# Kernel optimization log

Hardware: AMD Instinct MI355X
Metric: run time of the kernel (lower is better)

Reference implementation:

```python
import jax, jax.numpy as jnp
import numpy as np

B, C, T = 32, 256, 4096

def setup_inputs() -> dict:
    key = jax.random.key(0)
    k1, k2 = jax.random.split(key)
    x = jax.random.normal(k1, (B, C, T), dtype=jnp.float32)
    gamma = jax.random.normal(k2, (1,), dtype=jnp.float32)
    return {"x": x, "gamma": gamma}

def reference(x, gamma):
    # energy[b,i,j] = <x[b,i,:], x[b,j,:]>  -> (B, C, C)
    energy = jnp.einsum('bit,bjt->bij', x, x)
    # max-subtract trick: softmax over (rowmax - energy)
    energy_new = jnp.max(energy, axis=-1, keepdims=True) - energy
    attention = jax.nn.softmax(energy_new, axis=-1)
    # out[b,i,t] = sum_j attention[b,i,j] * x[b,j,t]
    out = jnp.einsum('bij,bjt->bit', attention, x)
    return gamma * out + x
```

## Files before the change

### kernel.cpp

```cpp
#include <hip/hip_runtime.h>
#include <hip/hip_bf16.h>

#define BATCH 32
#define CDIM  256
#define TDIM  4096

using short8  = __attribute__((ext_vector_type(8))) short;
using floatx4 = __attribute__((ext_vector_type(4))) float;
typedef unsigned short u16;

__device__ __forceinline__ unsigned f2bf(float f) {
  unsigned u = __float_as_uint(f);
  return (u + 0x7fffu + ((u >> 16) & 1u)) >> 16;
}
__device__ __forceinline__ unsigned cvt_pk_bf16(float a, float b) {
  return f2bf(a) | (f2bf(b) << 16);
}
__device__ __forceinline__ float bf_lo(unsigned u) { return __uint_as_float(u << 16); }
__device__ __forceinline__ float bf_hi(unsigned u) { return __uint_as_float(u & 0xffff0000u); }

__device__ __forceinline__ void glds16(const void* g, void* l) {
  __builtin_amdgcn_global_load_lds(
      (const __attribute__((address_space(1))) void*)g,
      (__attribute__((address_space(3))) void*)l, 16, 0, 0);
}

__global__ __launch_bounds__(256)
void split_kernel(const float* __restrict__ x, u16* __restrict__ hx,
                  u16* __restrict__ lx) {
  const unsigned gid0 = blockIdx.x * 256 + threadIdx.x;
#pragma unroll
  for (int it = 0; it < 8; ++it) {
    const size_t g8 = ((size_t)gid0 + (size_t)it * (2048u * 256u)) * 8;
    const float4 a = *(const float4*)(x + g8);
    const float4 c = *(const float4*)(x + g8 + 4);
    unsigned h0 = cvt_pk_bf16(a.x, a.y), h1 = cvt_pk_bf16(a.z, a.w);
    unsigned h2 = cvt_pk_bf16(c.x, c.y), h3 = cvt_pk_bf16(c.z, c.w);
    unsigned l0 = cvt_pk_bf16(a.x - bf_lo(h0), a.y - bf_hi(h0));
    unsigned l1 = cvt_pk_bf16(a.z - bf_lo(h1), a.w - bf_hi(h1));
    unsigned l2 = cvt_pk_bf16(c.x - bf_lo(h2), c.y - bf_hi(h2));
    unsigned l3 = cvt_pk_bf16(c.z - bf_lo(h3), c.w - bf_hi(h3));
    *(uint4*)(hx + g8) = make_uint4(h0, h1, h2, h3);
    *(uint4*)(lx + g8) = make_uint4(l0, l1, l2, l3);
  }
}

__global__ __launch_bounds__(512, 1)
void gram_gemm(const u16* __restrict__ hx, const u16* __restrict__ lx,
               float* __restrict__ S, float* __restrict__ E2) {
  __shared__ __align__(16) short lds[2 * 20480];

  const int tid = threadIdx.x;
  const int bx  = blockIdx.x;

  const int s8  = bx & 7;
  const int seq = bx >> 3;
  const int b   = s8 + ((seq >> 3) << 3);
  const int job = seq & 7;
  const int i0  = (job >> 2) << 7;
  const int j0  = (job & 3) << 6;

  const int lane = tid & 63;
  const int w    = tid >> 6;

  const int rsub = lane >> 3;
  const int gsw  = ((lane & 7) ^ rsub) << 3;
  const size_t xb = (size_t)b << 20;
  const u16* src[5];
  src[0] = hx + xb + (size_t)(i0 +      w * 8 + rsub) * TDIM + gsw;
  src[1] = hx + xb + (size_t)(i0 + 64 + w * 8 + rsub) * TDIM + gsw;
  src[2] = lx + xb + (size_t)(i0 +      w * 8 + rsub) * TDIM + gsw;
  src[3] = lx + xb + (size_t)(i0 + 64 + w * 8 + rsub) * TDIM + gsw;
  src[4] = hx + xb + (size_t)(j0 +      w * 8 + rsub) * TDIM + gsw;
  int dstoff[5];
#pragma unroll
  for (int s = 0; s < 5; ++s) dstoff[s] = (s * 8 + w) << 9;

  floatx4 acc1[2][2], acc2[2][2];
#pragma unroll
  for (int m = 0; m < 2; ++m)
#pragma unroll
    for (int n = 0; n < 2; ++n) {
      acc1[m][n] = {0.f, 0.f, 0.f, 0.f};
      acc2[m][n] = {0.f, 0.f, 0.f, 0.f};
    }

  const int wib = (w >> 1) << 5;
  const int wjb = (w & 1) << 5;
  const int fr  = lane & 15;
  const int q   = lane >> 4;
  const int f7  = fr & 7;

  const int g0 = ((q)     ^ f7) << 3;
  const int g1 = ((q + 4) ^ f7) << 3;
  const int a0 = (wib + fr) << 6;
  const int a1 = a0 + (16 << 6);
  const int b0 = (wjb + fr) << 6;
  const int b1 = b0 + (16 << 6);

#pragma unroll
  for (int s = 0; s < 5; ++s) glds16(src[s], lds + dstoff[s]);
  __syncthreads();

  for (int ks = 0; ks < 64; ++ks) {
    const int cur = ks & 1;
    if (ks < 63) {
      const int nb = (cur ^ 1) * 20480;
#pragma unroll
      for (int s = 0; s < 5; ++s)
        glds16(src[s] + ((ks + 1) << 6), lds + nb + dstoff[s]);
    }
    const int bb = cur * 20480;

    {
      short8 Ah0 = *(const short8*)&lds[bb + a0 + g0];
      short8 Ah1 = *(const short8*)&lds[bb + a1 + g0];
      short8 Al0 = *(const short8*)&lds[bb + 8192 + a0 + g0];
      short8 Al1 = *(const short8*)&lds[bb + 8192 + a1 + g0];
      short8 Bh0 = *(const short8*)&lds[bb + 16384 + b0 + g0];
      short8 Bh1 = *(const short8*)&lds[bb + 16384 + b1 + g0];
      acc1[0][0] = __builtin_amdgcn_mfma_f32_16x16x32_bf16(Ah0, Bh0, acc1[0][0], 0, 0, 0);
      acc1[0][1] = __builtin_amdgcn_mfma_f32_16x16x32_bf16(Ah0, Bh1, acc1[0][1], 0, 0, 0);
      acc1[1][0] = __builtin_amdgcn_mfma_f32_16x16x32_bf16(Ah1, Bh0, acc1[1][0], 0, 0, 0);
      acc1[1][1] = __builtin_amdgcn_mfma_f32_16x16x32_bf16(Ah1, Bh1, acc1[1][1], 0, 0, 0);
      acc2[0][0] = __builtin_amdgcn_mfma_f32_16x16x32_bf16(Al0, Bh0, acc2[0][0], 0, 0, 0);
      acc2[0][1] = __builtin_amdgcn_mfma_f32_16x16x32_bf16(Al0, Bh1, acc2[0][1], 0, 0, 0);
      acc2[1][0] = __builtin_amdgcn_mfma_f32_16x16x32_bf16(Al1, Bh0, acc2[1][0], 0, 0, 0);
      acc2[1][1] = __builtin_amdgcn_mfma_f32_16x16x32_bf16(Al1, Bh1, acc2[1][1], 0, 0, 0);
    }
    {
      short8 Ah0 = *(const short8*)&lds[bb + a0 + g1];
      short8 Ah1 = *(const short8*)&lds[bb + a1 + g1];
      short8 Al0 = *(const short8*)&lds[bb + 8192 + a0 + g1];
      short8 Al1 = *(const short8*)&lds[bb + 8192 + a1 + g1];
      short8 Bh0 = *(const short8*)&lds[bb + 16384 + b0 + g1];
      short8 Bh1 = *(const short8*)&lds[bb + 16384 + b1 + g1];
      acc1[0][0] = __builtin_amdgcn_mfma_f32_16x16x32_bf16(Ah0, Bh0, acc1[0][0], 0, 0, 0);
      acc1[0][1] = __builtin_amdgcn_mfma_f32_16x16x32_bf16(Ah0, Bh1, acc1[0][1], 0, 0, 0);
      acc1[1][0] = __builtin_amdgcn_mfma_f32_16x16x32_bf16(Ah1, Bh0, acc1[1][0], 0, 0, 0);
      acc1[1][1] = __builtin_amdgcn_mfma_f32_16x16x32_bf16(Ah1, Bh1, acc1[1][1], 0, 0, 0);
      acc2[0][0] = __builtin_amdgcn_mfma_f32_16x16x32_bf16(Al0, Bh0, acc2[0][0], 0, 0, 0);
      acc2[0][1] = __builtin_amdgcn_mfma_f32_16x16x32_bf16(Al0, Bh1, acc2[0][1], 0, 0, 0);
      acc2[1][0] = __builtin_amdgcn_mfma_f32_16x16x32_bf16(Al1, Bh0, acc2[1][0], 0, 0, 0);
      acc2[1][1] = __builtin_amdgcn_mfma_f32_16x16x32_bf16(Al1, Bh1, acc2[1][1], 0, 0, 0);
    }
    __syncthreads();
  }

#pragma unroll
  for (int m = 0; m < 2; ++m)
#pragma unroll
    for (int n = 0; n < 2; ++n) {
      const int gr = i0 + wib + 16 * m + 4 * q;
      const int gc = j0 + wjb + 16 * n + fr;
      size_t base = (((size_t)b * CDIM + gr) << 8) + gc;
#pragma unroll
      for (int r = 0; r < 4; ++r) {
        S[base + ((size_t)r << 8)]  = acc1[m][n][r] + acc2[m][n][r];
        E2[base + ((size_t)r << 8)] = acc2[m][n][r];
      }
    }
}

__global__ __launch_bounds__(512, 1)
void gram_fused(const float* __restrict__ x,
                float* __restrict__ S, float* __restrict__ E2) {
  __shared__ __align__(16) short hI[128 * 64];
  __shared__ __align__(16) short lI[128 * 64];
  __shared__ __align__(16) short hJ[64 * 64];

  const int tid = threadIdx.x;
  const int bx  = blockIdx.x;
  const int s   = bx & 7;
  const int seq = bx >> 3;
  const int b   = s + ((seq >> 3) << 3);
  const int job = seq & 7;
  const int i0  = (job >> 2) << 7;
  const int j0  = (job & 3) << 6;

  const float* xb = x + ((size_t)b << 20);

  const bool isJ   = tid >= 256;
  const int  irow  = tid >> 1;
  const int  ihalf = tid & 1;
  const int  jrow  = (tid & 255) >> 2;
  const int  jq    = tid & 3;

  const float* pS = isJ
      ? xb + (size_t)(j0 + jrow) * TDIM + (jq << 4)
      : xb + (size_t)(i0 + irow) * TDIM + (ihalf << 5);

  floatx4 acc1[2][2], acc2[2][2];
#pragma unroll
  for (int m = 0; m < 2; ++m)
#pragma unroll
    for (int n = 0; n < 2; ++n) {
      acc1[m][n] = {0.f, 0.f, 0.f, 0.f};
      acc2[m][n] = {0.f, 0.f, 0.f, 0.f};
    }

  const int lane = tid & 63;
  const int w    = tid >> 6;
  const int wib  = (w >> 1) << 5;
  const int wjb  = (w & 1) << 5;
  const int fr   = lane & 15;
  const int q    = lane >> 4;
  const int f7   = fr & 7;

  const int g0 = ((q)     ^ f7) << 3;
  const int g1 = ((q + 4) ^ f7) << 3;
  const int a0 = (wib + fr) << 6;
  const int a1 = a0 + (16 << 6);
  const int b0 = (wjb + fr) << 6;
  const int b1 = b0 + (16 << 6);

  float4 r0, r1, r2, r3, r4, r5, r6, r7;
  r0 = ((const float4*)pS)[0]; r1 = ((const float4*)pS)[1];
  r2 = ((const float4*)pS)[2]; r3 = ((const float4*)pS)[3];
  if (!isJ) {
    r4 = ((const float4*)pS)[4]; r5 = ((const float4*)pS)[5];
    r6 = ((const float4*)pS)[6]; r7 = ((const float4*)pS)[7];
  }

  for (int ks = 0; ks < TDIM / 64; ++ks) {
    unsigned h0 = cvt_pk_bf16(r0.x, r0.y), h1 = cvt_pk_bf16(r0.z, r0.w);
    unsigned h2 = cvt_pk_bf16(r1.x, r1.y), h3 = cvt_pk_bf16(r1.z, r1.w);
    unsigned h4 = cvt_pk_bf16(r2.x, r2.y), h5 = cvt_pk_bf16(r2.z, r2.w);
    unsigned h6 = cvt_pk_bf16(r3.x, r3.y), h7 = cvt_pk_bf16(r3.z, r3.w);
    unsigned h8, h9, hA, hB, hC, hD, hE, hF;
    unsigned l0, l1, l2, l3, l4, l5, l6, l7, l8, l9, lA, lB, lC, lD, lE, lF;
    if (!isJ) {
      h8 = cvt_pk_bf16(r4.x, r4.y); h9 = cvt_pk_bf16(r4.z, r4.w);
      hA = cvt_pk_bf16(r5.x, r5.y); hB = cvt_pk_bf16(r5.z, r5.w);
      hC = cvt_pk_bf16(r6.x, r6.y); hD = cvt_pk_bf16(r6.z, r6.w);
      hE = cvt_pk_bf16(r7.x, r7.y); hF = cvt_pk_bf16(r7.z, r7.w);
      l0 = cvt_pk_bf16(r0.x - bf_lo(h0), r0.y - bf_hi(h0));
      l1 = cvt_pk_bf16(r0.z - bf_lo(h1), r0.w - bf_hi(h1));
      l2 = cvt_pk_bf16(r1.x - bf_lo(h2), r1.y - bf_hi(h2));
      l3 = cvt_pk_bf16(r1.z - bf_lo(h3), r1.w - bf_hi(h3));
      l4 = cvt_pk_bf16(r2.x - bf_lo(h4), r2.y - bf_hi(h4));
      l5 = cvt_pk_bf16(r2.z - bf_lo(h5), r2.w - bf_hi(h5));
      l6 = cvt_pk_bf16(r3.x - bf_lo(h6), r3.y - bf_hi(h6));
      l7 = cvt_pk_bf16(r3.z - bf_lo(h7), r3.w - bf_hi(h7));
      l8 = cvt_pk_bf16(r4.x - bf_lo(h8), r4.y - bf_hi(h8));
      l9 = cvt_pk_bf16(r4.z - bf_lo(h9), r4.w - bf_hi(h9));
      lA = cvt_pk_bf16(r5.x - bf_lo(hA), r5.y - bf_hi(hA));
      lB = cvt_pk_bf16(r5.z - bf_lo(hB), r5.w - bf_hi(hB));
      lC = cvt_pk_bf16(r6.x - bf_lo(hC), r6.y - bf_hi(hC));
      lD = cvt_pk_bf16(r6.z - bf_lo(hD), r6.w - bf_hi(hD));
      lE = cvt_pk_bf16(r7.x - bf_lo(hE), r7.y - bf_hi(hE));
      lF = cvt_pk_bf16(r7.z - bf_lo(hF), r7.w - bf_hi(hF));
    }

    __syncthreads();
    if (!isJ) {
      const int rb = irow << 6;
      const int s7 = irow & 7;
      const int gb = ihalf << 2;
      *(uint4*)&hI[rb + (((gb + 0) ^ s7) << 3)] = make_uint4(h0, h1, h2, h3);
      *(uint4*)&hI[rb + (((gb + 1) ^ s7) << 3)] = make_uint4(h4, h5, h6, h7);
      *(uint4*)&hI[rb + (((gb + 2) ^ s7) << 3)] = make_uint4(h8, h9, hA, hB);
      *(uint4*)&hI[rb + (((gb + 3) ^ s7) << 3)] = make_uint4(hC, hD, hE, hF);
      *(uint4*)&lI[rb + (((gb + 0) ^ s7) << 3)] = make_uint4(l0, l1, l2, l3);
      *(uint4*)&lI[rb + (((gb + 1) ^ s7) << 3)] = make_uint4(l4, l5, l6, l7);
      *(uint4*)&lI[rb + (((gb + 2) ^ s7) << 3)] = make_uint4(l8, l9, lA, lB);
      *(uint4*)&lI[rb + (((gb + 3) ^ s7) << 3)] = make_uint4(lC, lD, lE, lF);
    } else {
      const int rb = jrow << 6;
      const int s7 = jrow & 7;
      const int gb = jq << 1;
      *(uint4*)&hJ[rb + (((gb + 0) ^ s7) << 3)] = make_uint4(h0, h1, h2, h3);
      *(uint4*)&hJ[rb + (((gb + 1) ^ s7) << 3)] = make_uint4(h4, h5, h6, h7);
    }
    __syncthreads();

    if (ks < TDIM / 64 - 1) {
      pS += 64;
      r0 = ((const float4*)pS)[0]; r1 = ((const float4*)pS)[1];
      r2 = ((const float4*)pS)[2]; r3 = ((const float4*)pS)[3];
      if (!isJ) {
        r4 = ((const float4*)pS)[4]; r5 = ((const float4*)pS)[5];
        r6 = ((const float4*)pS)[6]; r7 = ((const float4*)pS)[7];
      }
    }

    {
      short8 Ah0 = *(const short8*)&hI[a0 + g0];
      short8 Ah1 = *(const short8*)&hI[a1 + g0];
      short8 Al0 = *(const short8*)&lI[a0 + g0];
      short8 Al1 = *(const short8*)&lI[a1 + g0];
      short8 Bh0 = *(const short8*)&hJ[b0 + g0];
      short8 Bh1 = *(const short8*)&hJ[b1 + g0];
      acc1[0][0] = __builtin_amdgcn_mfma_f32_16x16x32_bf16(Ah0, Bh0, acc1[0][0], 0, 0, 0);
      acc1[0][1] = __builtin_amdgcn_mfma_f32_16x16x32_bf16(Ah0, Bh1, acc1[0][1], 0, 0, 0);
      acc1[1][0] = __builtin_amdgcn_mfma_f32_16x16x32_bf16(Ah1, Bh0, acc1[1][0], 0, 0, 0);
      acc1[1][1] = __builtin_amdgcn_mfma_f32_16x16x32_bf16(Ah1, Bh1, acc1[1][1], 0, 0, 0);
      acc2[0][0] = __builtin_amdgcn_mfma_f32_16x16x32_bf16(Al0, Bh0, acc2[0][0], 0, 0, 0);
      acc2[0][1] = __builtin_amdgcn_mfma_f32_16x16x32_bf16(Al0, Bh1, acc2[0][1], 0, 0, 0);
      acc2[1][0] = __builtin_amdgcn_mfma_f32_16x16x32_bf16(Al1, Bh0, acc2[1][0], 0, 0, 0);
      acc2[1][1] = __builtin_amdgcn_mfma_f32_16x16x32_bf16(Al1, Bh1, acc2[1][1], 0, 0, 0);
    }
    {
      short8 Ah0 = *(const short8*)&hI[a0 + g1];
      short8 Ah1 = *(const short8*)&hI[a1 + g1];
      short8 Al0 = *(const short8*)&lI[a0 + g1];
      short8 Al1 = *(const short8*)&lI[a1 + g1];
      short8 Bh0 = *(const short8*)&hJ[b0 + g1];
      short8 Bh1 = *(const short8*)&hJ[b1 + g1];
      acc1[0][0] = __builtin_amdgcn_mfma_f32_16x16x32_bf16(Ah0, Bh0, acc1[0][0], 0, 0, 0);
      acc1[0][1] = __builtin_amdgcn_mfma_f32_16x16x32_bf16(Ah0, Bh1, acc1[0][1], 0, 0, 0);
      acc1[1][0] = __builtin_amdgcn_mfma_f32_16x16x32_bf16(Ah1, Bh0, acc1[1][0], 0, 0, 0);
      acc1[1][1] = __builtin_amdgcn_mfma_f32_16x16x32_bf16(Ah1, Bh1, acc1[1][1], 0, 0, 0);
      acc2[0][0] = __builtin_amdgcn_mfma_f32_16x16x32_bf16(Al0, Bh0, acc2[0][0], 0, 0, 0);
      acc2[0][1] = __builtin_amdgcn_mfma_f32_16x16x32_bf16(Al0, Bh1, acc2[0][1], 0, 0, 0);
      acc2[1][0] = __builtin_amdgcn_mfma_f32_16x16x32_bf16(Al1, Bh0, acc2[1][0], 0, 0, 0);
      acc2[1][1] = __builtin_amdgcn_mfma_f32_16x16x32_bf16(Al1, Bh1, acc2[1][1], 0, 0, 0);
    }
  }

#pragma unroll
  for (int m = 0; m < 2; ++m)
#pragma unroll
    for (int n = 0; n < 2; ++n) {
      const int gr = i0 + wib + 16 * m + 4 * q;
      const int gc = j0 + wjb + 16 * n + fr;
      size_t base = (((size_t)b * CDIM + gr) << 8) + gc;
#pragma unroll
      for (int r = 0; r < 4; ++r) {
        S[base + ((size_t)r << 8)]  = acc1[m][n][r] + acc2[m][n][r];
        E2[base + ((size_t)r << 8)] = acc2[m][n][r];
      }
    }
}

__global__ __launch_bounds__(256)
void softmax_kernel(const float* __restrict__ S, const float* __restrict__ E2,
                    __hip_bfloat16* __restrict__ att) {
  __shared__ float SR[32][264];
  __shared__ float ST[256][33];

  const int tid = threadIdx.x;
  const int b   = blockIdx.x >> 3;
  const int i0  = (blockIdx.x & 7) << 5;
  const size_t base = (size_t)b << 16;

  {
    const int r  = tid >> 3;
    const int c0 = (tid & 7) << 5;
    const float* p1 = S + base + ((size_t)(i0 + r) << 8) + c0;
#pragma unroll
    for (int u = 0; u < 32; u += 4)
      *(float4*)&SR[r][c0 + u] = *(const float4*)(p1 + u);
  }
  {
    const int c  = tid & 31;
    const int j0 = (tid >> 5) << 5;
    const float* p = E2 + base + i0 + c;
#pragma unroll
    for (int jj = 0; jj < 32; ++jj)
      ST[j0 + jj][c] = p[(size_t)(j0 + jj) << 8];
  }
  __syncthreads();

  const int r  = tid >> 3;
  const int t7 = tid & 7;
  float z[32];
  float m = -3.4e38f;
#pragma unroll
  for (int k = 0; k < 32; ++k) {
    const int j = t7 + (k << 3);
    const float e = SR[r][j] + ST[j][r];
    z[k] = -e;
    m = fmaxf(m, z[k]);
  }
  m = fmaxf(m, __shfl_xor(m, 1, 64));
  m = fmaxf(m, __shfl_xor(m, 2, 64));
  m = fmaxf(m, __shfl_xor(m, 4, 64));
  float ssum = 0.f;
#pragma unroll
  for (int k = 0; k < 32; ++k) { z[k] = expf(z[k] - m); ssum += z[k]; }
  ssum += __shfl_xor(ssum, 1, 64);
  ssum += __shfl_xor(ssum, 2, 64);
  ssum += __shfl_xor(ssum, 4, 64);
  const float inv = 1.f / ssum;

  u16* arow = (u16*)att + base + ((size_t)(i0 + r) << 8);
#pragma unroll
  for (int k = 0; k < 32; ++k) {
    const int j = t7 + (k << 3);
    arow[j] = (u16)f2bf(z[k] * inv);
  }
}

__global__ __launch_bounds__(256, 1)
void pv_kernel(const float* __restrict__ x, const u16* __restrict__ hx,
               const __hip_bfloat16* __restrict__ att,
               const float* __restrict__ gamma, float* __restrict__ out) {
  __shared__ __align__(16) short As[128 * 256];
  __shared__ __align__(16) short Bs[128 * 256];

  const int tid = threadIdx.x;
  const int bx  = blockIdx.x;
  const int b   = bx >> 6;
  const int i0  = ((bx >> 5) & 1) << 7;
  const int t0  = (bx & 31) << 7;

  const u16* attb = (const u16*)att + ((size_t)b << 16) + ((size_t)i0 << 8);
  const int lane = tid & 63;
  const int w4   = tid >> 6;

  const int tQ = tid & 31;
  const int jg = tid >> 5;
  const u16* hb = hx + ((size_t)b << 20) + t0 + (tQ << 2);
  uint2 v[4][8];
#pragma unroll
  for (int j8 = 0; j8 < 4; ++j8)
#pragma unroll
    for (int u = 0; u < 8; ++u)
      v[j8][u] = *(const uint2*)(hb + (size_t)((jg << 5) + (j8 << 3) + u) * TDIM);

#pragma unroll
  for (int s = 0; s < 16; ++s) {
    const int c  = (s << 2) + w4;
    const int r  = (c << 1) + (lane >> 5);
    const int gd = lane & 31;
    const int gs = gd ^ (r & 7);
    glds16(attb + ((size_t)r << 8) + (gs << 3), As + (c << 9));
  }

#pragma unroll
  for (int j8 = 0; j8 < 4; ++j8) {
#pragma unroll
    for (int tt = 0; tt < 4; ++tt) {
      unsigned p[4];
#pragma unroll
      for (int a = 0; a < 4; ++a) {
        const unsigned xa = (tt & 2) ? v[j8][2 * a].y : v[j8][2 * a].x;
        const unsigned xb2 = (tt & 2) ? v[j8][2 * a + 1].y : v[j8][2 * a + 1].x;
        p[a] = (tt & 1) ? ((xa >> 16) | (xb2 & 0xffff0000u))
                        : ((xa & 0xffffu) | (xb2 << 16));
      }
      const int row = (tQ << 2) + tt;
      const int g   = ((jg << 2) + j8) ^ (row & 7);
      *(uint4*)(Bs + row * 256 + (g << 3)) = make_uint4(p[0], p[1], p[2], p[3]);
    }
  }

  floatx4 acc[4][4];
#pragma unroll
  for (int m = 0; m < 4; ++m)
#pragma unroll
    for (int n = 0; n < 4; ++n) acc[m][n] = {0.f, 0.f, 0.f, 0.f};

  const int wm = (w4 >> 1) << 6;
  const int wn = (w4 & 1) << 6;
  const int fr = lane & 15;
  const int q  = lane >> 4;

  __syncthreads();

#pragma unroll
  for (int ks = 0; ks < 8; ++ks) {
    short8 Af[4], Bf[4];
#pragma unroll
    for (int m = 0; m < 4; ++m) {
      const int r = wm + 16 * m + fr;
      const int g = ((ks << 2) + q) ^ (r & 7);
      Af[m] = *(const short8*)(As + r * 256 + (g << 3));
    }
#pragma unroll
    for (int n = 0; n < 4; ++n) {
      const int r = wn + 16 * n + fr;
      const int g = ((ks << 2) + q) ^ (r & 7);
      Bf[n] = *(const short8*)(Bs + r * 256 + (g << 3));
    }
#pragma unroll
    for (int m = 0; m < 4; ++m)
#pragma unroll
      for (int n = 0; n < 4; ++n)
        acc[m][n] = __builtin_amdgcn_mfma_f32_16x16x32_bf16(Af[m], Bf[n], acc[m][n], 0, 0, 0);
  }

  const float g = gamma[0];
#pragma unroll
  for (int m = 0; m < 4; ++m)
#pragma unroll
    for (int n = 0; n < 4; ++n) {
      const int gr = i0 + wm + 16 * m + 4 * q;
      const int gc = t0 + wn + 16 * n + fr;
      size_t base = ((size_t)b << 20) + (size_t)gr * TDIM + gc;
#pragma unroll
      for (int r = 0; r < 4; ++r) {
        size_t idx = base + (size_t)r * TDIM;
        out[idx] = g * acc[m][n][r] + x[idx];
      }
    }
}

__global__ __launch_bounds__(256, 1)
void pv_fused(const float* __restrict__ x, const __hip_bfloat16* __restrict__ att,
              const float* __restrict__ gamma, float* __restrict__ out) {
  __shared__ __align__(16) short As[128 * 256];
  __shared__ __align__(16) short Bs[128 * 256];

  const int tid = threadIdx.x;
  const int bx  = blockIdx.x;
  const int b   = bx >> 6;
  const int i0  = ((bx >> 5) & 1) << 7;
  const int t0  = (bx & 31) << 7;

  const float* xb = x + ((size_t)b << 20) + t0;
  const u16* attb = (const u16*)att + ((size_t)b << 16) + ((size_t)i0 << 8);

  {
    uint4 areg[16];
#pragma unroll
    for (int c = 0; c < 16; ++c) {
      const int p = (c << 8) + tid;
      const int r = p >> 5;
      const int g = (p & 31) ^ (r & 7);
      areg[c] = *(const uint4*)(attb + (r << 8) + (g << 3));
    }
#pragma unroll
    for (int c = 0; c < 16; ++c) {
      const int p = (c << 8) + tid;
      *(uint4*)((char*)As + ((size_t)p << 4)) = areg[c];
    }
  }
  {
    const int tQ = tid & 31;
    const int jg = tid >> 5;
#pragma unroll
    for (int j8 = 0; j8 < 4; ++j8) {
      floatx4 v[8];
#pragma unroll
      for (int u = 0; u < 8; ++u) {
        const int j = (jg << 5) + (j8 << 3) + u;
        v[u] = *(const floatx4*)(xb + (size_t)j * TDIM + (tQ << 2));
      }
#pragma unroll
      for (int tt = 0; tt < 4; ++tt) {
        uint4 wv = make_uint4(cvt_pk_bf16(v[0][tt], v[1][tt]),
                              cvt_pk_bf16(v[2][tt], v[3][tt]),
                              cvt_pk_bf16(v[4][tt], v[5][tt]),
                              cvt_pk_bf16(v[6][tt], v[7][tt]));
        const int row = (tQ << 2) + tt;
        const int g   = ((jg << 2) + j8) ^ (row & 7);
        *(uint4*)((char*)Bs + (size_t)row * 512 + ((size_t)g << 4)) = wv;
      }
    }
  }

  floatx4 acc[4][4];
#pragma unroll
  for (int m = 0; m < 4; ++m)
#pragma unroll
    for (int n = 0; n < 4; ++n) acc[m][n] = {0.f, 0.f, 0.f, 0.f};

  const int lane = tid & 63;
  const int w    = tid >> 6;
  const int wm   = (w >> 1) << 6;
  const int wn   = (w & 1) << 6;
  const int fr   = lane & 15;
  const int q    = lane >> 4;

  __syncthreads();

#pragma unroll
  for (int ks = 0; ks < 8; ++ks) {
    short8 Af[4], Bf[4];
#pragma unroll
    for (int m = 0; m < 4; ++m) {
      const int r = wm + 16 * m + fr;
      const int g = ((ks << 2) + q) ^ (r & 7);
      Af[m] = *(const short8*)((char*)As + (size_t)r * 512 + ((size_t)g << 4));
    }
#pragma unroll
    for (int n = 0; n < 4; ++n) {
      const int r = wn + 16 * n + fr;
      const int g = ((ks << 2) + q) ^ (r & 7);
      Bf[n] = *(const short8*)((char*)Bs + (size_t)r * 512 + ((size_t)g << 4));
    }
#pragma unroll
    for (int m = 0; m < 4; ++m)
#pragma unroll
      for (int n = 0; n < 4; ++n)
        acc[m][n] = __builtin_amdgcn_mfma_f32_16x16x32_bf16(Af[m], Bf[n], acc[m][n], 0, 0, 0);
  }

  const float g = gamma[0];
#pragma unroll
  for (int m = 0; m < 4; ++m)
#pragma unroll
    for (int n = 0; n < 4; ++n) {
      const int gr = i0 + wm + 16 * m + 4 * q;
      const int gc = t0 + wn + 16 * n + fr;
      size_t base = ((size_t)b << 20) + (size_t)gr * TDIM + gc;
#pragma unroll
      for (int r = 0; r < 4; ++r) {
        size_t idx = base + (size_t)r * TDIM;
        out[idx] = g * acc[m][n][r] + x[idx];
      }
    }
}

extern "C" void kernel_launch(void* const* d_in, const int* in_sizes, int n_in,
                              void* d_out, int out_size, void* d_ws, size_t ws_size,
                              hipStream_t stream) {
  (void)in_sizes; (void)n_in; (void)out_size;
  const float* x     = (const float*)d_in[0];
  const float* gamma = (const float*)d_in[1];
  float* out = (float*)d_out;

  const size_t EN = (size_t)BATCH * CDIM * CDIM;
  const size_t XN = (size_t)BATCH * CDIM * TDIM;
  float* S  = (float*)d_ws;
  float* E2 = S + EN;
  __hip_bfloat16* att = (__hip_bfloat16*)(E2 + EN);
  u16* hx = (u16*)((char*)d_ws + 20u * 1024 * 1024);
  u16* lx = hx + XN;
  const size_t need = 20u * 1024 * 1024 + 2 * XN * sizeof(u16);

  if (ws_size >= need) {
    split_kernel<<<dim3(2048), dim3(256), 0, stream>>>(x, hx, lx);
    gram_gemm<<<dim3(256), dim3(512), 0, stream>>>(hx, lx, S, E2);
    softmax_kernel<<<dim3(BATCH * 8), dim3(256), 0, stream>>>(S, E2, att);
    pv_kernel<<<dim3(2048), dim3(256), 0, stream>>>(x, hx, att, gamma, out);
  } else {
    gram_fused<<<dim3(256), dim3(512), 0, stream>>>(x, S, E2);
    softmax_kernel<<<dim3(BATCH * 8), dim3(256), 0, stream>>>(S, E2, att);
    pv_fused<<<dim3(2048), dim3(256), 0, stream>>>(x, att, gamma, out);
  }
}
```

Baseline: 371.3 us.

## Precompute transposed bf16 x for PV and relax gram_gemm barriers

```diff
diff --git a/kernel.cpp b/kernel.cpp
--- a/kernel.cpp
+++ b/kernel.cpp
@@ -23,6 +23,54 @@
   __builtin_amdgcn_global_load_lds(
       (const __attribute__((address_space(1))) void*)g,
       (__attribute__((address_space(3))) void*)l, 16, 0, 0);
+}
+
+__global__ __launch_bounds__(256)
+void split_t_kernel(const float* __restrict__ x, u16* __restrict__ hx,
+                    u16* __restrict__ lx, u16* __restrict__ hxT) {
+  __shared__ u16 ht[64][72];
+
+  const int bx  = blockIdx.x;
+  const int b   = bx >> 8;
+  const int j0  = ((bx >> 6) & 3) << 6;
+  const int t0  = (bx & 63) << 6;
+  const int tid = threadIdx.x;
+  const int jr  = tid >> 2;
+  const int tc  = (tid & 3) << 4;
+
+  const size_t xoff = ((size_t)b << 20) + (size_t)(j0 + jr) * TDIM + t0 + tc;
+  const float4 a0 = ((const float4*)(x + xoff))[0];
+  const float4 a1 = ((const float4*)(x + xoff))[1];
+  const float4 a2 = ((const float4*)(x + xoff))[2];
+  const float4 a3 = ((const float4*)(x + xoff))[3];
+  const float4 aa[4] = {a0, a1, a2, a3};
+
+  unsigned h[8], l[8];
+#pragma unroll
+  for (int u = 0; u < 4; ++u) {
+    h[2 * u]     = cvt_pk_bf16(aa[u].x, aa[u].y);
+    h[2 * u + 1] = cvt_pk_bf16(aa[u].z, aa[u].w);
+    l[2 * u]     = cvt_pk_bf16(aa[u].x - bf_lo(h[2 * u]),     aa[u].y - bf_hi(h[2 * u]));
+    l[2 * u + 1] = cvt_pk_bf16(aa[u].z - bf_lo(h[2 * u + 1]), aa[u].w - bf_hi(h[2 * u + 1]));
+  }
+
+  u16* ph = hx + xoff;
+  *(uint4*)ph       = make_uint4(h[0], h[1], h[2], h[3]);
+  *(uint4*)(ph + 8) = make_uint4(h[4], h[5], h[6], h[7]);
+  u16* pl = lx + xoff;
+  *(uint4*)pl       = make_uint4(l[0], l[1], l[2], l[3]);
+  *(uint4*)(pl + 8) = make_uint4(l[4], l[5], l[6], l[7]);
+
+#pragma unroll
+  for (int u = 0; u < 16; ++u)
+    ht[tc + u][jr] = (u16)((u & 1) ? (h[u >> 1] >> 16) : (h[u >> 1] & 0xffffu));
+  __syncthreads();
+
+  const int tr = tid >> 2;
+  const int jc = (tid & 3) << 4;
+  u16* pt = hxT + ((size_t)b << 20) + (size_t)(t0 + tr) * CDIM + j0 + jc;
+  *(uint4*)pt       = *(const uint4*)&ht[tr][jc];
+  *(uint4*)(pt + 8) = *(const uint4*)&ht[tr][jc + 8];
 }
 
 __global__ __launch_bounds__(256)
@@ -100,17 +148,19 @@
 
 #pragma unroll
   for (int s = 0; s < 5; ++s) glds16(src[s], lds + dstoff[s]);
-  __syncthreads();
 
   for (int ks = 0; ks < 64; ++ks) {
-    const int cur = ks & 1;
+    const int bb = (ks & 1) * 20480;
     if (ks < 63) {
-      const int nb = (cur ^ 1) * 20480;
+      const int nb = ((ks + 1) & 1) * 20480;
 #pragma unroll
       for (int s = 0; s < 5; ++s)
         glds16(src[s] + ((ks + 1) << 6), lds + nb + dstoff[s]);
-    }
-    const int bb = cur * 20480;
+      asm volatile("s_waitcnt vmcnt(5)" ::: "memory");
+    } else {
+      asm volatile("s_waitcnt vmcnt(0)" ::: "memory");
+    }
+    __builtin_amdgcn_s_barrier();
 
     {
       short8 Ah0 = *(const short8*)&lds[bb + a0 + g0];
@@ -144,7 +194,8 @@
       acc2[1][0] = __builtin_amdgcn_mfma_f32_16x16x32_bf16(Al1, Bh0, acc2[1][0], 0, 0, 0);
       acc2[1][1] = __builtin_amdgcn_mfma_f32_16x16x32_bf16(Al1, Bh1, acc2[1][1], 0, 0, 0);
     }
-    __syncthreads();
+    asm volatile("" ::: "memory");
+    __builtin_amdgcn_s_barrier();
   }
 
 #pragma unroll
@@ -240,6 +291,7 @@
       l3 = cvt_pk_bf16(r1.z - bf_lo(h3), r1.w - bf_hi(h3));
       l4 = cvt_pk_bf16(r2.x - bf_lo(h4), r2.y - bf_hi(h4));
       l5 = cvt_pk_bf16(r2.z - bf_lo(h5), r2.w - bf_hi(h5));
+      l6 = cvt_pk_bf16(r3.x - bf_lo(h6), r3.w - bf_hi(h6));
       l6 = cvt_pk_bf16(r3.x - bf_lo(h6), r3.y - bf_hi(h6));
       l7 = cvt_pk_bf16(r3.z - bf_lo(h7), r3.w - bf_hi(h7));
       l8 = cvt_pk_bf16(r4.x - bf_lo(h8), r4.y - bf_hi(h8));
@@ -392,8 +444,8 @@
   }
 }
 
-__global__ __launch_bounds__(256, 1)
-void pv_kernel(const float* __restrict__ x, const u16* __restrict__ hx,
+__global__ __launch_bounds__(512, 1)
+void pv_kernel(const float* __restrict__ x, const u16* __restrict__ hxT,
                const __hip_bfloat16* __restrict__ att,
                const float* __restrict__ gamma, float* __restrict__ out) {
   __shared__ __align__(16) short As[128 * 256];
@@ -405,55 +457,37 @@
   const int i0  = ((bx >> 5) & 1) << 7;
   const int t0  = (bx & 31) << 7;
 
-  const u16* attb = (const u16*)att + ((size_t)b << 16) + ((size_t)i0 << 8);
+  const u16* asrc = (const u16*)att + ((size_t)b << 16) + ((size_t)i0 << 8);
+  const u16* bsrc = hxT + ((size_t)b << 20) + ((size_t)t0 << 8);
+
   const int lane = tid & 63;
-  const int w4   = tid >> 6;
-
-  const int tQ = tid & 31;
-  const int jg = tid >> 5;
-  const u16* hb = hx + ((size_t)b << 20) + t0 + (tQ << 2);
-  uint2 v[4][8];
-#pragma unroll
-  for (int j8 = 0; j8 < 4; ++j8)
-#pragma unroll
-    for (int u = 0; u < 8; ++u)
-      v[j8][u] = *(const uint2*)(hb + (size_t)((jg << 5) + (j8 << 3) + u) * TDIM);
-
-#pragma unroll
-  for (int s = 0; s < 16; ++s) {
-    const int c  = (s << 2) + w4;
-    const int r  = (c << 1) + (lane >> 5);
-    const int gd = lane & 31;
+  const int w    = tid >> 6;
+
+  const int rh = lane >> 5;
+  const int gd = lane & 31;
+#pragma unroll
+  for (int s = 0; s < 8; ++s) {
+    const int c  = (s << 3) + w;
+    const int r  = (c << 1) + rh;
     const int gs = gd ^ (r & 7);
-    glds16(attb + ((size_t)r << 8) + (gs << 3), As + (c << 9));
-  }
-
-#pragma unroll
-  for (int j8 = 0; j8 < 4; ++j8) {
-#pragma unroll
-    for (int tt = 0; tt < 4; ++tt) {
-      unsigned p[4];
-#pragma unroll
-      for (int a = 0; a < 4; ++a) {
-        const unsigned xa = (tt & 2) ? v[j8][2 * a].y : v[j8][2 * a].x;
-        const unsigned xb2 = (tt & 2) ? v[j8][2 * a + 1].y : v[j8][2 * a + 1].x;
-        p[a] = (tt & 1) ? ((xa >> 16) | (xb2 & 0xffff0000u))
-                        : ((xa & 0xffffu) | (xb2 << 16));
-      }
-      const int row = (tQ << 2) + tt;
-      const int g   = ((jg << 2) + j8) ^ (row & 7);
-      *(uint4*)(Bs + row * 256 + (g << 3)) = make_uint4(p[0], p[1], p[2], p[3]);
-    }
-  }
-
-  floatx4 acc[4][4];
+    glds16(asrc + ((size_t)r << 8) + (gs << 3), As + (c << 9));
+  }
+#pragma unroll
+  for (int s = 0; s < 8; ++s) {
+    const int c  = (s << 3) + w;
+    const int r  = (c << 1) + rh;
+    const int gs = gd ^ (r & 7);
+    glds16(bsrc + ((size_t)r << 8) + (gs << 3), Bs + (c << 9));
+  }
+
+  floatx4 acc[4][2];
 #pragma unroll
   for (int m = 0; m < 4; ++m)
 #pragma unroll
-    for (int n = 0; n < 4; ++n) acc[m][n] = {0.f, 0.f, 0.f, 0.f};
-
-  const int wm = (w4 >> 1) << 6;
-  const int wn = (w4 & 1) << 6;
+    for (int n = 0; n < 2; ++n) acc[m][n] = {0.f, 0.f, 0.f, 0.f};
+
+  const int wm = (w >> 2) << 6;
+  const int wn = (w & 3) << 5;
   const int fr = lane & 15;
   const int q  = lane >> 4;
 
@@ -461,7 +495,7 @@
 
 #pragma unroll
   for (int ks = 0; ks < 8; ++ks) {
-    short8 Af[4], Bf[4];
+    short8 Af[4], Bf[2];
 #pragma unroll
     for (int m = 0; m < 4; ++m) {
       const int r = wm + 16 * m + fr;
@@ -469,7 +503,7 @@
       Af[m] = *(const short8*)(As + r * 256 + (g << 3));
     }
 #pragma unroll
-    for (int n = 0; n < 4; ++n) {
+    for (int n = 0; n < 2; ++n) {
       const int r = wn + 16 * n + fr;
       const int g = ((ks << 2) + q) ^ (r & 7);
       Bf[n] = *(const short8*)(Bs + r * 256 + (g << 3));
@@ -477,7 +511,7 @@
 #pragma unroll
     for (int m = 0; m < 4; ++m)
 #pragma unroll
-      for (int n = 0; n < 4; ++n)
+      for (int n = 0; n < 2; ++n)
         acc[m][n] = __builtin_amdgcn_mfma_f32_16x16x32_bf16(Af[m], Bf[n], acc[m][n], 0, 0, 0);
   }
 
@@ -485,7 +519,7 @@
 #pragma unroll
   for (int m = 0; m < 4; ++m)
 #pragma unroll
-    for (int n = 0; n < 4; ++n) {
+    for (int n = 0; n < 2; ++n) {
       const int gr = i0 + wm + 16 * m + 4 * q;
       const int gc = t0 + wn + 16 * n + fr;
       size_t base = ((size_t)b << 20) + (size_t)gr * TDIM + gc;
@@ -545,8 +579,8 @@
                               cvt_pk_bf16(v[4][tt], v[5][tt]),
                               cvt_pk_bf16(v[6][tt], v[7][tt]));
         const int row = (tQ << 2) + tt;
-        const int g   = ((jg << 2) + j8) ^ (row & 7);
-        *(uint4*)((char*)Bs + (size_t)row * 512 + ((size_t)g << 4)) = wv;
+        const int gx  = ((jg << 2) + j8) ^ (row & 7);
+        *(uint4*)((char*)Bs + (size_t)row * 512 + ((size_t)gx << 4)) = wv;
       }
     }
   }
@@ -612,20 +646,28 @@
   const float* gamma = (const float*)d_in[1];
   float* out = (float*)d_out;
 
+  const size_t MB = 1024 * 1024;
   const size_t EN = (size_t)BATCH * CDIM * CDIM;
   const size_t XN = (size_t)BATCH * CDIM * TDIM;
   float* S  = (float*)d_ws;
   float* E2 = S + EN;
   __hip_bfloat16* att = (__hip_bfloat16*)(E2 + EN);
-  u16* hx = (u16*)((char*)d_ws + 20u * 1024 * 1024);
-  u16* lx = hx + XN;
-  const size_t need = 20u * 1024 * 1024 + 2 * XN * sizeof(u16);
-
-  if (ws_size >= need) {
+  u16* hx  = (u16*)((char*)d_ws + 20 * MB);
+  u16* lx  = hx + XN;
+  u16* hxT = lx + XN;
+  const size_t need_full = 20 * MB + 3 * XN * sizeof(u16);
+  const size_t need_mid  = 20 * MB + 2 * XN * sizeof(u16);
+
+  if (ws_size >= need_full) {
+    split_t_kernel<<<dim3(8192), dim3(256), 0, stream>>>(x, hx, lx, hxT);
+    gram_gemm<<<dim3(256), dim3(512), 0, stream>>>(hx, lx, S, E2);
+    softmax_kernel<<<dim3(BATCH * 8), dim3(256), 0, stream>>>(S, E2, att);
+    pv_kernel<<<dim3(2048), dim3(512), 0, stream>>>(x, hxT, att, gamma, out);
+  } else if (ws_size >= need_mid) {
     split_kernel<<<dim3(2048), dim3(256), 0, stream>>>(x, hx, lx);
     gram_gemm<<<dim3(256), dim3(512), 0, stream>>>(hx, lx, S, E2);
     softmax_kernel<<<dim3(BATCH * 8), dim3(256), 0, stream>>>(S, E2, att);
-    pv_kernel<<<dim3(2048), dim3(256), 0, stream>>>(x, hx, att, gamma, out);
+    pv_fused<<<dim3(2048), dim3(256), 0, stream>>>(x, att, gamma, out);
   } else {
     gram_fused<<<dim3(256), dim3(512), 0, stream>>>(x, S, E2);
     softmax_kernel<<<dim3(BATCH * 8), dim3(256), 0, stream>>>(S, E2, att);
```

Result: slower. 403.9 us (+8.8%).

## Shrink gram and PV tiles, add triple-buffered async prefetch in gram GEMM

Applied to the files above, without the earlier changes.

```diff
diff --git a/kernel.cpp b/kernel.cpp
--- a/kernel.cpp
+++ b/kernel.cpp
@@ -45,19 +45,19 @@
   }
 }
 
-__global__ __launch_bounds__(512, 1)
+__global__ __launch_bounds__(256, 2)
 void gram_gemm(const u16* __restrict__ hx, const u16* __restrict__ lx,
                float* __restrict__ S, float* __restrict__ E2) {
-  __shared__ __align__(16) short lds[2 * 20480];
+  __shared__ __align__(16) short lds[3 * 12288];
 
   const int tid = threadIdx.x;
   const int bx  = blockIdx.x;
 
   const int s8  = bx & 7;
   const int seq = bx >> 3;
-  const int b   = s8 + ((seq >> 3) << 3);
-  const int job = seq & 7;
-  const int i0  = (job >> 2) << 7;
+  const int b   = s8 + ((seq >> 4) << 3);
+  const int job = seq & 15;
+  const int i0  = (job >> 2) << 6;
   const int j0  = (job & 3) << 6;
 
   const int lane = tid & 63;
@@ -66,15 +66,19 @@
   const int rsub = lane >> 3;
   const int gsw  = ((lane & 7) ^ rsub) << 3;
   const size_t xb = (size_t)b << 20;
-  const u16* src[5];
-  src[0] = hx + xb + (size_t)(i0 +      w * 8 + rsub) * TDIM + gsw;
-  src[1] = hx + xb + (size_t)(i0 + 64 + w * 8 + rsub) * TDIM + gsw;
-  src[2] = lx + xb + (size_t)(i0 +      w * 8 + rsub) * TDIM + gsw;
-  src[3] = lx + xb + (size_t)(i0 + 64 + w * 8 + rsub) * TDIM + gsw;
-  src[4] = hx + xb + (size_t)(j0 +      w * 8 + rsub) * TDIM + gsw;
-  int dstoff[5];
-#pragma unroll
-  for (int s = 0; s < 5; ++s) dstoff[s] = (s * 8 + w) << 9;
+  const u16* src[6];
+  int dstoff[6];
+#pragma unroll
+  for (int s = 0; s < 6; ++s) {
+    const int c = (s << 2) + w;
+    const u16* base;
+    int row;
+    if (c < 8)       { base = hx; row = i0 + (c << 3) + rsub; }
+    else if (c < 16) { base = lx; row = i0 + ((c - 8) << 3) + rsub; }
+    else             { base = hx; row = j0 + ((c - 16) << 3) + rsub; }
+    src[s]    = base + xb + (size_t)row * TDIM + gsw;
+    dstoff[s] = c << 9;
+  }
 
   floatx4 acc1[2][2], acc2[2][2];
 #pragma unroll
@@ -99,26 +103,33 @@
   const int b1 = b0 + (16 << 6);
 
 #pragma unroll
-  for (int s = 0; s < 5; ++s) glds16(src[s], lds + dstoff[s]);
-  __syncthreads();
+  for (int s = 0; s < 6; ++s) glds16(src[s], lds + dstoff[s]);
+#pragma unroll
+  for (int s = 0; s < 6; ++s) glds16(src[s] + 64, lds + 12288 + dstoff[s]);
+
+  int cur = 0;
+  int nx2 = 2 * 12288;
 
   for (int ks = 0; ks < 64; ++ks) {
-    const int cur = ks & 1;
-    if (ks < 63) {
-      const int nb = (cur ^ 1) * 20480;
-#pragma unroll
-      for (int s = 0; s < 5; ++s)
-        glds16(src[s] + ((ks + 1) << 6), lds + nb + dstoff[s]);
-    }
-    const int bb = cur * 20480;
+    if (ks < 62) {
+#pragma unroll
+      for (int s = 0; s < 6; ++s)
+        glds16(src[s] + ((ks + 2) << 6), lds + nx2 + dstoff[s]);
+      asm volatile("s_waitcnt vmcnt(12)" ::: "memory");
+    } else if (ks == 62) {
+      asm volatile("s_waitcnt vmcnt(6)" ::: "memory");
+    } else {
+      asm volatile("s_waitcnt vmcnt(0)" ::: "memory");
+    }
+    __builtin_amdgcn_s_barrier();
 
     {
-      short8 Ah0 = *(const short8*)&lds[bb + a0 + g0];
-      short8 Ah1 = *(const short8*)&lds[bb + a1 + g0];
-      short8 Al0 = *(const short8*)&lds[bb + 8192 + a0 + g0];
-      short8 Al1 = *(const short8*)&lds[bb + 8192 + a1 + g0];
-      short8 Bh0 = *(const short8*)&lds[bb + 16384 + b0 + g0];
-      short8 Bh1 = *(const short8*)&lds[bb + 16384 + b1 + g0];
+      short8 Ah0 = *(const short8*)&lds[cur + a0 + g0];
+      short8 Ah1 = *(const short8*)&lds[cur + a1 + g0];
+      short8 Al0 = *(const short8*)&lds[cur + 4096 + a0 + g0];
+      short8 Al1 = *(const short8*)&lds[cur + 4096 + a1 + g0];
+      short8 Bh0 = *(const short8*)&lds[cur + 8192 + b0 + g0];
+      short8 Bh1 = *(const short8*)&lds[cur + 8192 + b1 + g0];
       acc1[0][0] = __builtin_amdgcn_mfma_f32_16x16x32_bf16(Ah0, Bh0, acc1[0][0], 0, 0, 0);
       acc1[0][1] = __builtin_amdgcn_mfma_f32_16x16x32_bf16(Ah0, Bh1, acc1[0][1], 0, 0, 0);
       acc1[1][0] = __builtin_amdgcn_mfma_f32_16x16x32_bf16(Ah1, Bh0, acc1[1][0], 0, 0, 0);
@@ -129,12 +140,12 @@
       acc2[1][1] = __builtin_amdgcn_mfma_f32_16x16x32_bf16(Al1, Bh1, acc2[1][1], 0, 0, 0);
     }
     {
-      short8 Ah0 = *(const short8*)&lds[bb + a0 + g1];
-      short8 Ah1 = *(const short8*)&lds[bb + a1 + g1];
-      short8 Al0 = *(const short8*)&lds[bb + 8192 + a0 + g1];
-      short8 Al1 = *(const short8*)&lds[bb + 8192 + a1 + g1];
-      short8 Bh0 = *(const short8*)&lds[bb + 16384 + b0 + g1];
-      short8 Bh1 = *(const short8*)&lds[bb + 16384 + b1 + g1];
+      short8 Ah0 = *(const short8*)&lds[cur + a0 + g1];
+      short8 Ah1 = *(const short8*)&lds[cur + a1 + g1];
+      short8 Al0 = *(const short8*)&lds[cur + 4096 + a0 + g1];
+      short8 Al1 = *(const short8*)&lds[cur + 4096 + a1 + g1];
+      short8 Bh0 = *(const short8*)&lds[cur + 8192 + b0 + g1];
+      short8 Bh1 = *(const short8*)&lds[cur + 8192 + b1 + g1];
       acc1[0][0] = __builtin_amdgcn_mfma_f32_16x16x32_bf16(Ah0, Bh0, acc1[0][0], 0, 0, 0);
       acc1[0][1] = __builtin_amdgcn_mfma_f32_16x16x32_bf16(Ah0, Bh1, acc1[0][1], 0, 0, 0);
       acc1[1][0] = __builtin_amdgcn_mfma_f32_16x16x32_bf16(Ah1, Bh0, acc1[1][0], 0, 0, 0);
@@ -144,7 +155,11 @@
       acc2[1][0] = __builtin_amdgcn_mfma_f32_16x16x32_bf16(Al1, Bh0, acc2[1][0], 0, 0, 0);
       acc2[1][1] = __builtin_amdgcn_mfma_f32_16x16x32_bf16(Al1, Bh1, acc2[1][1], 0, 0, 0);
     }
-    __syncthreads();
+    asm volatile("" ::: "memory");
+    __builtin_amdgcn_s_barrier();
+
+    cur += 12288; if (cur == 36864) cur = 0;
+    nx2 += 12288; if (nx2 == 36864) nx2 = 0;
   }
 
 #pragma unroll
@@ -392,68 +407,67 @@
   }
 }
 
-__global__ __launch_bounds__(256, 1)
+__global__ __launch_bounds__(256, 2)
 void pv_kernel(const float* __restrict__ x, const u16* __restrict__ hx,
                const __hip_bfloat16* __restrict__ att,
                const float* __restrict__ gamma, float* __restrict__ out) {
-  __shared__ __align__(16) short As[128 * 256];
-  __shared__ __align__(16) short Bs[128 * 256];
+  __shared__ __align__(16) short As[64 * 256];
+  __shared__ __align__(16) short Bs[64 * 256];
 
   const int tid = threadIdx.x;
   const int bx  = blockIdx.x;
-  const int b   = bx >> 6;
-  const int i0  = ((bx >> 5) & 1) << 7;
-  const int t0  = (bx & 31) << 7;
-
-  const u16* attb = (const u16*)att + ((size_t)b << 16) + ((size_t)i0 << 8);
+  const int b   = bx >> 8;
+  const int i0  = ((bx >> 6) & 3) << 6;
+  const int t0  = (bx & 63) << 6;
+
+  const u16* asrc = (const u16*)att + ((size_t)b << 16) + ((size_t)i0 << 8);
   const int lane = tid & 63;
-  const int w4   = tid >> 6;
-
-  const int tQ = tid & 31;
-  const int jg = tid >> 5;
+  const int w    = tid >> 6;
+
+  const int tQ = tid & 15;
+  const int jg = tid >> 4;
   const u16* hb = hx + ((size_t)b << 20) + t0 + (tQ << 2);
-  uint2 v[4][8];
-#pragma unroll
-  for (int j8 = 0; j8 < 4; ++j8)
+  uint2 v[2][8];
+#pragma unroll
+  for (int j8 = 0; j8 < 2; ++j8)
 #pragma unroll
     for (int u = 0; u < 8; ++u)
-      v[j8][u] = *(const uint2*)(hb + (size_t)((jg << 5) + (j8 << 3) + u) * TDIM);
-
-#pragma unroll
-  for (int s = 0; s < 16; ++s) {
-    const int c  = (s << 2) + w4;
+      v[j8][u] = *(const uint2*)(hb + (size_t)((jg << 4) + (j8 << 3) + u) * TDIM);
+
+#pragma unroll
+  for (int s = 0; s < 8; ++s) {
+    const int c  = (s << 2) + w;
     const int r  = (c << 1) + (lane >> 5);
-    const int gd = lane & 31;
-    const int gs = gd ^ (r & 7);
-    glds16(attb + ((size_t)r << 8) + (gs << 3), As + (c << 9));
-  }
-
-#pragma unroll
-  for (int j8 = 0; j8 < 4; ++j8) {
+    const int gs = (lane & 31) ^ (r & 7);
+    glds16(asrc + ((size_t)r << 8) + (gs << 3), As + (c << 9));
+  }
+
+#pragma unroll
+  for (int j8 = 0; j8 < 2; ++j8) {
 #pragma unroll
     for (int tt = 0; tt < 4; ++tt) {
       unsigned p[4];
 #pragma unroll
       for (int a = 0; a < 4; ++a) {
-        const unsigned xa = (tt & 2) ? v[j8][2 * a].y : v[j8][2 * a].x;
+        const unsigned xa  = (tt & 2) ? v[j8][2 * a].y : v[j8][2 * a].x;
         const unsigned xb2 = (tt & 2) ? v[j8][2 * a + 1].y : v[j8][2 * a + 1].x;
         p[a] = (tt & 1) ? ((xa >> 16) | (xb2 & 0xffff0000u))
                         : ((xa & 0xffffu) | (xb2 << 16));
       }
       const int row = (tQ << 2) + tt;
-      const int g   = ((jg << 2) + j8) ^ (row & 7);
+      const int g   = ((jg << 1) + j8) ^ (row & 7);
       *(uint4*)(Bs + row * 256 + (g << 3)) = make_uint4(p[0], p[1], p[2], p[3]);
     }
   }
 
-  floatx4 acc[4][4];
-#pragma unroll
-  for (int m = 0; m < 4; ++m)
-#pragma unroll
-    for (int n = 0; n < 4; ++n) acc[m][n] = {0.f, 0.f, 0.f, 0.f};
-
-  const int wm = (w4 >> 1) << 6;
-  const int wn = (w4 & 1) << 6;
+  floatx4 acc[2][2];
+#pragma unroll
+  for (int m = 0; m < 2; ++m)
+#pragma unroll
+    for (int n = 0; n < 2; ++n) acc[m][n] = {0.f, 0.f, 0.f, 0.f};
+
+  const int wm = (w >> 1) << 5;
+  const int wn = (w & 1) << 5;
   const int fr = lane & 15;
   const int q  = lane >> 4;
 
@@ -461,31 +475,31 @@
 
 #pragma unroll
   for (int ks = 0; ks < 8; ++ks) {
-    short8 Af[4], Bf[4];
-#pragma unroll
-    for (int m = 0; m < 4; ++m) {
+    short8 Af[2], Bf[2];
+#pragma unroll
+    for (int m = 0; m < 2; ++m) {
       const int r = wm + 16 * m + fr;
       const int g = ((ks << 2) + q) ^ (r & 7);
       Af[m] = *(const short8*)(As + r * 256 + (g << 3));
     }
 #pragma unroll
-    for (int n = 0; n < 4; ++n) {
+    for (int n = 0; n < 2; ++n) {
       const int r = wn + 16 * n + fr;
       const int g = ((ks << 2) + q) ^ (r & 7);
       Bf[n] = *(const short8*)(Bs + r * 256 + (g << 3));
     }
 #pragma unroll
-    for (int m = 0; m < 4; ++m)
-#pragma unroll
-      for (int n = 0; n < 4; ++n)
+    for (int m = 0; m < 2; ++m)
+#pragma unroll
+      for (int n = 0; n < 2; ++n)
         acc[m][n] = __builtin_amdgcn_mfma_f32_16x16x32_bf16(Af[m], Bf[n], acc[m][n], 0, 0, 0);
   }
 
   const float g = gamma[0];
 #pragma unroll
-  for (int m = 0; m < 4; ++m)
-#pragma unroll
-    for (int n = 0; n < 4; ++n) {
+  for (int m = 0; m < 2; ++m)
+#pragma unroll
+    for (int n = 0; n < 2; ++n) {
       const int gr = i0 + wm + 16 * m + 4 * q;
       const int gc = t0 + wn + 16 * n + fr;
       size_t base = ((size_t)b << 20) + (size_t)gr * TDIM + gc;
@@ -545,8 +559,8 @@
                               cvt_pk_bf16(v[4][tt], v[5][tt]),
                               cvt_pk_bf16(v[6][tt], v[7][tt]));
         const int row = (tQ << 2) + tt;
-        const int g   = ((jg << 2) + j8) ^ (row & 7);
-        *(uint4*)((char*)Bs + (size_t)row * 512 + ((size_t)g << 4)) = wv;
+        const int gx  = ((jg << 2) + j8) ^ (row & 7);
+        *(uint4*)((char*)Bs + (size_t)row * 512 + ((size_t)gx << 4)) = wv;
       }
     }
   }
@@ -612,20 +626,21 @@
   const float* gamma = (const float*)d_in[1];
   float* out = (float*)d_out;
 
+  const size_t MB = 1024 * 1024;
   const size_t EN = (size_t)BATCH * CDIM * CDIM;
   const size_t XN = (size_t)BATCH * CDIM * TDIM;
   float* S  = (float*)d_ws;
   float* E2 = S + EN;
   __hip_bfloat16* att = (__hip_bfloat16*)(E2 + EN);
-  u16* hx = (u16*)((char*)d_ws + 20u * 1024 * 1024);
-  u16* lx = hx + XN;
-  const size_t need = 20u * 1024 * 1024 + 2 * XN * sizeof(u16);
+  u16* hx  = (u16*)((char*)d_ws + 20 * MB);
+  u16* lx  = hx + XN;
+  const size_t need = 20 * MB + 2 * XN * sizeof(u16);
 
   if (ws_size >= need) {
     split_kernel<<<dim3(2048), dim3(256), 0, stream>>>(x, hx, lx);
-    gram_gemm<<<dim3(256), dim3(512), 0, stream>>>(hx, lx, S, E2);
+    gram_gemm<<<dim3(512), dim3(256), 0, stream>>>(hx, lx, S, E2);
     softmax_kernel<<<dim3(BATCH * 8), dim3(256), 0, stream>>>(S, E2, att);
-    pv_kernel<<<dim3(2048), dim3(256), 0, stream>>>(x, hx, att, gamma, out);
+    pv_kernel<<<dim3(8192), dim3(256), 0, stream>>>(x, hx, att, gamma, out);
   } else {
     gram_fused<<<dim3(256), dim3(512), 0, stream>>>(x, S, E2);
     softmax_kernel<<<dim3(BATCH * 8), dim3(256), 0, stream>>>(S, E2, att);
```

New measurement: 367.9 us. About the same (-0.9%).
